# Kernel tuning notes

Measured on AMD Instinct MI355X. Metric: run time of the kernel, lower is better.

## Reference

```python
import jax, jax.numpy as jnp
import numpy as np

DIM = 512
HEADS = 8
DIM_HEAD = 64
INNER = HEADS * DIM_HEAD  # 512
SCALE = DIM_HEAD ** -0.5
NEG = -jnp.finfo(jnp.float32).max


def setup_inputs() -> dict:
    key = jax.random.key(0)
    k1, k2, k3, k4, k5 = jax.random.split(key, 5)
    b, n = 2, 4096
    x = jax.random.normal(k1, (b, n, DIM), dtype=jnp.float32)
    mask = jnp.ones((b, n), dtype=bool)
    gamma = jnp.ones((DIM,), dtype=jnp.float32)
    # nn.Linear default init ~ U(-1/sqrt(fan_in), 1/sqrt(fan_in)); use scaled normal for simplicity
    Wq = jax.random.normal(k2, (DIM, INNER), dtype=jnp.float32) * (DIM ** -0.5)
    Wkv = jax.random.normal(k3, (DIM, 2 * INNER), dtype=jnp.float32) * (DIM ** -0.5)
    Wout = jax.random.normal(k4, (INNER, DIM), dtype=jnp.float32) * (INNER ** -0.5)
    return {"x": x, "mask": mask, "gamma": gamma, "Wq": Wq, "Wkv": Wkv, "Wout": Wout}


def _layer_norm(x, gamma):
    mu = jnp.mean(x, axis=-1, keepdims=True)
    var = jnp.var(x, axis=-1, keepdims=True)
    return (x - mu) * jax.lax.rsqrt(var + 1e-5) * gamma  # beta buffer is zeros


def reference(x, mask, gamma, Wq, Wkv, Wout):
    b, n, _ = x.shape
    xn = _layer_norm(x, gamma)
    q = xn @ Wq                      # [b,n,inner]
    kv = xn @ Wkv                    # [b,n,2*inner]
    k, v = jnp.split(kv, 2, axis=-1)
    # b n (h d) -> b h n d
    def split_heads(t):
        return t.reshape(b, n, HEADS, DIM_HEAD).transpose(0, 2, 1, 3)
    q, k, v = split_heads(q) * SCALE, split_heads(k), split_heads(v)
    sim = jnp.einsum('bhid,bhjd->bhij', q, k)  # [b,h,n,n]
    sim = jnp.where(mask[:, None, None, :], sim, NEG)
    causal = jnp.triu(jnp.ones((n, n), dtype=bool), k=1)
    sim = jnp.where(causal, NEG, sim)
    attn = jax.nn.softmax(sim, axis=-1)
    out = jnp.einsum('bhij,bhjd->bhid', attn, v)       # [b,h,n,d]
    out = out.transpose(0, 2, 1, 3).reshape(b, n, INNER)
    return out @ Wout
```

## Files before the change

kernel.cpp:

```cpp
#include <hip/hip_runtime.h>
#include <hip/hip_bf16.h>
#include <stdint.h>

typedef __attribute__((ext_vector_type(8))) short bf16x8;
typedef __attribute__((ext_vector_type(4))) float f32x4;
typedef __attribute__((ext_vector_type(16))) float f32x16;
typedef __attribute__((ext_vector_type(4))) uint32_t u32x4;

__device__ __forceinline__ short f2bf(float f) {
    union { float f; uint32_t u; } v; v.f = f;
    uint32_t r = v.u + 0x7fffu + ((v.u >> 16) & 1u);
    return (short)(r >> 16);
}

__device__ __forceinline__ float bf2f(uint32_t bits) {
    union { uint32_t u; float f; } v; v.u = bits;
    return v.f;
}

__device__ __forceinline__ uint32_t cvtpk(float a, float b) {
    uint32_t r;
    asm("v_cvt_pk_bf16_f32 %0, %1, %2" : "=v"(r) : "v"(a), "v"(b));
    return r;
}

__device__ __forceinline__ void plswap(uint32_t& x, uint32_t& y) {
    asm volatile("v_permlane32_swap_b32 %0, %1" : "+v"(x), "+v"(y));
}

__device__ __forceinline__ f32x16 mfma32(bf16x8 a, bf16x8 b, f32x16 c) {
    return __builtin_amdgcn_mfma_f32_32x32x16_bf16(a, b, c, 0, 0, 0);
}

__device__ __forceinline__ void gload_lds16(const void* g, void* l) {
    __builtin_amdgcn_global_load_lds(
        (const __attribute__((address_space(1))) void*)g,
        (__attribute__((address_space(3))) void*)l, 16, 0, 0);
}

__global__ __launch_bounds__(256) void prep_weights(
    const float* __restrict__ Wq, const float* __restrict__ Wkv,
    const float* __restrict__ Wout, short* __restrict__ WqkvT,
    short* __restrict__ WoutT) {
    int tid = blockIdx.x * 256 + threadIdx.x;
    if (tid < 1536 * 512) {
        int n = tid >> 9, k = tid & 511;
        float w = (n < 512) ? Wq[k * 512 + n] : Wkv[k * 1024 + (n - 512)];
        WqkvT[tid] = f2bf(w);
    } else {
        int t = tid - 1536 * 512;
        int n = t >> 9, k = t & 511;
        WoutT[t] = f2bf(Wout[k * 512 + n]);
    }
}

__global__ __launch_bounds__(256) void layernorm_k(
    const float* __restrict__ x, const float* __restrict__ gamma,
    short* __restrict__ xn) {
    int row = blockIdx.x;
    const float* xr = x + (size_t)row * 512;
    float2 v = *(const float2*)(xr + threadIdx.x * 2);
    float s = v.x + v.y;
    float ss = v.x * v.x + v.y * v.y;
#pragma unroll
    for (int off = 1; off < 64; off <<= 1) {
        s += __shfl_xor(s, off);
        ss += __shfl_xor(ss, off);
    }
    __shared__ float sbuf[4], ssbuf[4];
    int wid = threadIdx.x >> 6;
    if ((threadIdx.x & 63) == 0) { sbuf[wid] = s; ssbuf[wid] = ss; }
    __syncthreads();
    s = sbuf[0] + sbuf[1] + sbuf[2] + sbuf[3];
    ss = ssbuf[0] + ssbuf[1] + ssbuf[2] + ssbuf[3];
    float mu = s * (1.f / 512.f);
    float var = ss * (1.f / 512.f) - mu * mu;
    float rstd = rsqrtf(var + 1e-5f);
    float2 g = *(const float2*)(gamma + threadIdx.x * 2);
    uint32_t lo = (uint16_t)f2bf((v.x - mu) * rstd * g.x);
    uint32_t hi = (uint16_t)f2bf((v.y - mu) * rstd * g.y);
    *(uint32_t*)(xn + (size_t)row * 512 + threadIdx.x * 2) = lo | (hi << 16);
}

template <int EPI>
__global__ __launch_bounds__(256) void gemm_bt(const short* __restrict__ A,
                                               const short* __restrict__ Bt,
                                               void* __restrict__ C) {
    constexpr int K = 512;
    constexpr int CS = (EPI == 0) ? 1536 : 512;
    __shared__ __align__(16) short As[128 * 64];
    __shared__ __align__(16) short Bs[128 * 64];
    const int tid = threadIdx.x;
    const int lane = tid & 63;
    const int wid = tid >> 6;
    const int m0 = blockIdx.x * 128;
    const int n0 = blockIdx.y * 128;
    const int wr = wid >> 1, wc = wid & 1;
    const int hi = lane >> 4, lo = lane & 15;

    f32x4 acc[4][4] = {};
    for (int kt = 0; kt < K / 64; ++kt) {
        __syncthreads();
#pragma unroll
        for (int r = 0; r < 4; ++r) {
            int c = (r * 4 + wid) * 64 + lane;
            int row = c >> 3, c8 = c & 7;
            int kcol = kt * 64 + ((c8 ^ (row & 7)) << 3);
            gload_lds16(A + (size_t)(m0 + row) * K + kcol,
                        (char*)As + (r * 4 + wid) * 1024);
            gload_lds16(Bt + (size_t)(n0 + row) * K + kcol,
                        (char*)Bs + (r * 4 + wid) * 1024);
        }
        __syncthreads();
#pragma unroll
        for (int kk = 0; kk < 2; ++kk) {
            bf16x8 af[4], bfr[4];
            int cc = hi + kk * 4;
#pragma unroll
            for (int i = 0; i < 4; ++i) {
                int row = wr * 64 + i * 16 + lo;
                af[i] = *(const bf16x8*)((const char*)As + row * 128 +
                                         ((cc ^ (row & 7)) << 4));
                int nrow = wc * 64 + i * 16 + lo;
                bfr[i] = *(const bf16x8*)((const char*)Bs + nrow * 128 +
                                          ((cc ^ (nrow & 7)) << 4));
            }
#pragma unroll
            for (int i = 0; i < 4; ++i)
#pragma unroll
                for (int j = 0; j < 4; ++j)
                    acc[i][j] = __builtin_amdgcn_mfma_f32_16x16x32_bf16(
                        af[i], bfr[j], acc[i][j], 0, 0, 0);
        }
    }
#pragma unroll
    for (int i = 0; i < 4; ++i)
#pragma unroll
        for (int j = 0; j < 4; ++j) {
            int col = n0 + wc * 64 + j * 16 + lo;
#pragma unroll
            for (int r = 0; r < 4; ++r) {
                int row = m0 + wr * 64 + i * 16 + hi * 4 + r;
                float v = acc[i][j][r];
                if (EPI == 0) {
                    if (col < 512) v *= 0.18033688011112042f;
                    ((short*)C)[(size_t)row * CS + col] = f2bf(v);
                } else {
                    ((float*)C)[(size_t)row * CS + col] = v;
                }
            }
        }
}

__global__ __launch_bounds__(256) void transpose_v(const short* __restrict__ qkv,
                                                   short* __restrict__ Vt) {
    __shared__ __align__(16) short T[64 * 72];
    int tid = threadIdx.x;
    int bh = blockIdx.y, b = bh >> 3, h = bh & 7;
    int n0 = blockIdx.x * 64;
    const short* src = qkv + (size_t)(b * 4096 + n0) * 1536 + 1024 + h * 64;
#pragma unroll
    for (int r = 0; r < 2; ++r) {
        int c = r * 256 + tid;
        int t = c >> 3, d0 = (c & 7) * 8;
        *(bf16x8*)(&T[t * 72 + d0]) = *(const bf16x8*)(src + (size_t)t * 1536 + d0);
    }
    __syncthreads();
    short* dst = Vt + (size_t)bh * 64 * 4096 + n0;
#pragma unroll
    for (int r = 0; r < 2; ++r) {
        int c = r * 256 + tid;
        int d = c >> 3, tt0 = (c & 7) * 8;
        short o[8];
#pragma unroll
        for (int j = 0; j < 8; ++j) o[j] = T[(tt0 + j) * 72 + d];
        *(bf16x8*)(dst + (size_t)d * 4096 + tt0) = *(bf16x8*)o;
    }
}

__global__ __launch_bounds__(256, 4) void flash_attn(
    const short* __restrict__ qkv, const short* __restrict__ Vt,
    short* __restrict__ attn_out) {
    __shared__ __align__(16) char smem[32768];
    const int tid = threadIdx.x, lane = tid & 63, w = tid >> 6;
    const int hi32 = lane >> 5, lq = lane & 31;
    const int bid = blockIdx.x;
    const int qt = 127 - (bid >> 4);
    const int bh = bid & 15, b = bh >> 3, h = bh & 7;
    const int q0 = qt * 32;
    const int qg = q0 + lq;
    const int swzK = (lq & 7) ^ ((lq >> 3) & 1);
    const int swzV = (lq >> 1) & 3;

    bf16x8 qb[4];
    {
        const short* qrow = qkv + (size_t)(b * 4096 + qg) * 1536 + h * 64;
#pragma unroll
        for (int ks = 0; ks < 4; ++ks)
            qb[ks] = *(const bf16x8*)(qrow + ks * 16 + hi32 * 8);
    }

    const short* kptr = qkv + (size_t)b * 4096 * 1536 + 512 + h * 64;
    const short* vptr = Vt + (size_t)bh * 64 * 4096;
    char* mybuf = smem + w * 8192;

    auto stage = [&](int t) {
        const short* kp = kptr + (size_t)t * 32 * 1536;
        const short* vp = vptr + t * 32;
#pragma unroll
        for (int r = 0; r < 4; ++r) {
            int idx = r * 64 + lane;
            int krow = idx >> 3, kc = idx & 7;
            int ksw = (krow & 7) ^ ((krow >> 3) & 1);
            gload_lds16(kp + (size_t)krow * 1536 + ((kc ^ ksw) << 3),
                        mybuf + idx * 16);
            int vrow = idx >> 2, vc = idx & 3;
            int vcl = vc ^ ((vrow >> 1) & 3);
            gload_lds16(vp + (size_t)vrow * 4096 + (vcl << 3),
                        mybuf + 4096 + idx * 16);
        }
    };

    f32x16 oA = {}, oB = {};
    float m_r = -3.0e38f, l_r = 0.f;
    const int T = qt + 1;

    if (w < T) {
        stage(w);
        for (int t = w; t < T; t += 4) {
            asm volatile("s_waitcnt vmcnt(0)" ::: "memory");
            f32x16 sA = {};
            __builtin_amdgcn_s_setprio(1);
#pragma unroll
            for (int ks = 0; ks < 4; ++ks) {
                int p = (2 * ks + hi32) ^ swzK;
                bf16x8 kf = *(const bf16x8*)(mybuf + lq * 128 + p * 16);
                sA = mfma32(kf, qb[ks], sA);
            }
            __builtin_amdgcn_s_setprio(0);
            bf16x8 vfA[2], vfB[2];
#pragma unroll
            for (int ks = 0; ks < 2; ++ks) {
                int p = (2 * ks + hi32) ^ swzV;
                vfA[ks] = *(const bf16x8*)(mybuf + 4096 + lq * 64 + p * 16);
                vfB[ks] =
                    *(const bf16x8*)(mybuf + 4096 + (lq + 32) * 64 + p * 16);
            }
            asm volatile("s_waitcnt lgkmcnt(0)" ::: "memory");
            __builtin_amdgcn_sched_barrier(0);
            if (t + 4 < T) stage(t + 4);
            int kv0 = t * 32;
            if (kv0 + 31 > q0) {
                int c4 = 4 * hi32;
#pragma unroll
                for (int r2 = 0; r2 < 16; ++r2) {
                    int kvl = (r2 & 3) + 8 * (r2 >> 2) + c4;
                    sA[r2] = (kv0 + kvl > qg) ? -3.0e38f : sA[r2];
                }
            }
            float m0 = m_r, m1 = m_r, m2 = m_r, m3 = m_r;
#pragma unroll
            for (int r2 = 0; r2 < 16; r2 += 4) {
                m0 = fmaxf(sA[r2], m0);
                m1 = fmaxf(sA[r2 + 1], m1);
                m2 = fmaxf(sA[r2 + 2], m2);
                m3 = fmaxf(sA[r2 + 3], m3);
            }
            float mt = fmaxf(fmaxf(m0, m1), fmaxf(m2, m3));
            mt = fmaxf(mt, __shfl_xor(mt, 32));
            if (!__all(mt <= m_r + 8.0f)) {
                float alpha = exp2f(m_r - mt);
                m_r = mt;
                l_r *= alpha;
#pragma unroll
                for (int r2 = 0; r2 < 16; ++r2) {
                    oA[r2] *= alpha;
                    oB[r2] *= alpha;
                }
            }
            float sum0 = 0.f;
#pragma unroll
            for (int r2 = 0; r2 < 16; ++r2) {
                sA[r2] = exp2f(sA[r2] - m_r);
                sum0 += sA[r2];
            }
            float rs = sum0 + __shfl_xor(sum0, 32);
            l_r += rs;
#pragma unroll
            for (int ks = 0; ks < 2; ++ks) {
                const int base = ks * 8;
                uint32_t x0 = cvtpk(sA[base + 0], sA[base + 1]);
                uint32_t y0 = cvtpk(sA[base + 4], sA[base + 5]);
                plswap(x0, y0);
                uint32_t x1 = cvtpk(sA[base + 2], sA[base + 3]);
                uint32_t y1 = cvtpk(sA[base + 6], sA[base + 7]);
                plswap(x1, y1);
                union { uint32_t wd[4]; bf16x8 v; } u;
                u.wd[0] = x0; u.wd[1] = x1; u.wd[2] = y0; u.wd[3] = y1;
                __builtin_amdgcn_s_setprio(1);
                oA = mfma32(vfA[ks], u.v, oA);
                oB = mfma32(vfB[ks], u.v, oB);
                __builtin_amdgcn_s_setprio(0);
            }
        }
    }
    __syncthreads();
    {
        char* epi = smem + w * 4352;
        float invl = (l_r > 0.f) ? (1.0f / l_r) : 0.f;
#pragma unroll
        for (int r2 = 0; r2 < 16; r2 += 2) {
            int wbase = ((r2 & 3) >> 1) + 4 * (r2 >> 2) + 2 * hi32;
            *(uint32_t*)(epi + lq * 136 + wbase * 4) =
                cvtpk(oA[r2] * invl, oA[r2 + 1] * invl);
            *(uint32_t*)(epi + lq * 136 + 64 + wbase * 4) =
                cvtpk(oB[r2] * invl, oB[r2 + 1] * invl);
        }
        float* mlb = (float*)(smem + 17408);
        if (hi32 == 0) {
            mlb[w * 64 + lq] = m_r;
            mlb[w * 64 + 32 + lq] = l_r;
        }
    }
    __syncthreads();
    {
        const int q = tid >> 3, dg = tid & 7;
        const float* mlb = (const float*)(smem + 17408);
        float M = -3.0e38f;
        float mm[4], ll[4];
#pragma unroll
        for (int s = 0; s < 4; ++s) {
            mm[s] = mlb[s * 64 + q];
            ll[s] = mlb[s * 64 + 32 + q];
            M = fmaxf(M, mm[s]);
        }
        float L = 0.f;
        float acc[8] = {};
#pragma unroll
        for (int s = 0; s < 4; ++s) {
            float a = exp2f(mm[s] - M) * ll[s];
            L += a;
            u32x4 pv = *(const u32x4*)(smem + s * 4352 + q * 136 + dg * 16);
#pragma unroll
            for (int j = 0; j < 4; ++j) {
                acc[2 * j] += a * bf2f(pv[j] << 16);
                acc[2 * j + 1] += a * bf2f(pv[j] & 0xffff0000u);
            }
        }
        float inv = 1.0f / L;
        u32x4 o;
#pragma unroll
        for (int j = 0; j < 4; ++j)
            o[j] = cvtpk(acc[2 * j] * inv, acc[2 * j + 1] * inv);
        uint32_t* attn32 = (uint32_t*)attn_out;
        *(u32x4*)(attn32 + (size_t)(b * 4096 + q0 + q) * 256 + h * 32 + dg * 4) =
            o;
    }
}

extern "C" void kernel_launch(void* const* d_in, const int* in_sizes, int n_in,
                              void* d_out, int out_size, void* d_ws,
                              size_t ws_size, hipStream_t stream) {
    const float* x = (const float*)d_in[0];
    const float* gamma = (const float*)d_in[2];
    const float* Wq = (const float*)d_in[3];
    const float* Wkv = (const float*)d_in[4];
    const float* Wout = (const float*)d_in[5];

    char* ws = (char*)d_ws;
    short* xn = (short*)(ws);
    short* qkv = (short*)(ws + (8ull << 20));
    short* Vt = (short*)(ws + (32ull << 20));
    short* attn = (short*)(ws + (40ull << 20));
    short* WqkvT = (short*)(ws + (48ull << 20));
    short* WoutT = (short*)(ws + (50ull << 20));

    prep_weights<<<4096, 256, 0, stream>>>(Wq, Wkv, Wout, WqkvT, WoutT);
    layernorm_k<<<8192, 256, 0, stream>>>(x, gamma, xn);
    gemm_bt<0><<<dim3(64, 12), 256, 0, stream>>>(xn, WqkvT, qkv);
    transpose_v<<<dim3(64, 16), 256, 0, stream>>>(qkv, Vt);
    flash_attn<<<2048, 256, 0, stream>>>(qkv, Vt, attn);
    gemm_bt<1><<<dim3(64, 4), 256, 0, stream>>>(attn, WoutT, (float*)d_out);
}
```

Measured before the change: 133.7 us.

## Fuse layernorm with weight prep, write V transposed from QKV GEMM, streamline softmax

Merges weight conversion and layernorm into one launch, and has the QKV GEMM epilogue write V directly in transposed layout, which removes the separate transpose kernel and two launches. The attention kernel precomputes its staging offsets and seeds scores with the negated running max so the max subtraction folds into the MFMA accumulator init. It also restructures the online-softmax rescale and sum reductions and shrinks the epilogue LDS stride from 136 to 132 bytes. The transposed V stores are 8-byte scattered writes, which may be less coalesced than the old transpose kernel's output.

```diff
diff --git a/kernel.cpp b/kernel.cpp
--- a/kernel.cpp
+++ b/kernel.cpp
@@ -3,6 +3,7 @@
 #include <stdint.h>
 
 typedef __attribute__((ext_vector_type(8))) short bf16x8;
+typedef __attribute__((ext_vector_type(4))) short s16x4;
 typedef __attribute__((ext_vector_type(4))) float f32x4;
 typedef __attribute__((ext_vector_type(16))) float f32x16;
 typedef __attribute__((ext_vector_type(4))) uint32_t u32x4;
@@ -38,56 +39,55 @@
         (__attribute__((address_space(3))) void*)l, 16, 0, 0);
 }
 
-__global__ __launch_bounds__(256) void prep_weights(
+__global__ __launch_bounds__(256) void prep_ln(
+    const float* __restrict__ x, const float* __restrict__ gamma,
     const float* __restrict__ Wq, const float* __restrict__ Wkv,
-    const float* __restrict__ Wout, short* __restrict__ WqkvT,
-    short* __restrict__ WoutT) {
-    int tid = blockIdx.x * 256 + threadIdx.x;
-    if (tid < 1536 * 512) {
-        int n = tid >> 9, k = tid & 511;
-        float w = (n < 512) ? Wq[k * 512 + n] : Wkv[k * 1024 + (n - 512)];
-        WqkvT[tid] = f2bf(w);
+    const float* __restrict__ Wout, short* __restrict__ xn,
+    short* __restrict__ WqkvT, short* __restrict__ WoutT) {
+    if (blockIdx.x < 8192) {
+        int row = blockIdx.x;
+        const float* xr = x + (size_t)row * 512;
+        float2 v = *(const float2*)(xr + threadIdx.x * 2);
+        float s = v.x + v.y;
+        float ss = v.x * v.x + v.y * v.y;
+#pragma unroll
+        for (int off = 1; off < 64; off <<= 1) {
+            s += __shfl_xor(s, off);
+            ss += __shfl_xor(ss, off);
+        }
+        __shared__ float sbuf[4], ssbuf[4];
+        int wid = threadIdx.x >> 6;
+        if ((threadIdx.x & 63) == 0) { sbuf[wid] = s; ssbuf[wid] = ss; }
+        __syncthreads();
+        s = sbuf[0] + sbuf[1] + sbuf[2] + sbuf[3];
+        ss = ssbuf[0] + ssbuf[1] + ssbuf[2] + ssbuf[3];
+        float mu = s * (1.f / 512.f);
+        float var = ss * (1.f / 512.f) - mu * mu;
+        float rstd = rsqrtf(var + 1e-5f);
+        float2 g = *(const float2*)(gamma + threadIdx.x * 2);
+        uint32_t lo = (uint16_t)f2bf((v.x - mu) * rstd * g.x);
+        uint32_t hi = (uint16_t)f2bf((v.y - mu) * rstd * g.y);
+        *(uint32_t*)(xn + (size_t)row * 512 + threadIdx.x * 2) = lo | (hi << 16);
     } else {
-        int t = tid - 1536 * 512;
-        int n = t >> 9, k = t & 511;
-        WoutT[t] = f2bf(Wout[k * 512 + n]);
-    }
-}
-
-__global__ __launch_bounds__(256) void layernorm_k(
-    const float* __restrict__ x, const float* __restrict__ gamma,
-    short* __restrict__ xn) {
-    int row = blockIdx.x;
-    const float* xr = x + (size_t)row * 512;
-    float2 v = *(const float2*)(xr + threadIdx.x * 2);
-    float s = v.x + v.y;
-    float ss = v.x * v.x + v.y * v.y;
-#pragma unroll
-    for (int off = 1; off < 64; off <<= 1) {
-        s += __shfl_xor(s, off);
-        ss += __shfl_xor(ss, off);
-    }
-    __shared__ float sbuf[4], ssbuf[4];
-    int wid = threadIdx.x >> 6;
-    if ((threadIdx.x & 63) == 0) { sbuf[wid] = s; ssbuf[wid] = ss; }
-    __syncthreads();
-    s = sbuf[0] + sbuf[1] + sbuf[2] + sbuf[3];
-    ss = ssbuf[0] + ssbuf[1] + ssbuf[2] + ssbuf[3];
-    float mu = s * (1.f / 512.f);
-    float var = ss * (1.f / 512.f) - mu * mu;
-    float rstd = rsqrtf(var + 1e-5f);
-    float2 g = *(const float2*)(gamma + threadIdx.x * 2);
-    uint32_t lo = (uint16_t)f2bf((v.x - mu) * rstd * g.x);
-    uint32_t hi = (uint16_t)f2bf((v.y - mu) * rstd * g.y);
-    *(uint32_t*)(xn + (size_t)row * 512 + threadIdx.x * 2) = lo | (hi << 16);
+        int tid = (blockIdx.x - 8192) * 256 + threadIdx.x;
+        if (tid < 1536 * 512) {
+            int n = tid >> 9, k = tid & 511;
+            float w = (n < 512) ? Wq[k * 512 + n] : Wkv[k * 1024 + (n - 512)];
+            WqkvT[tid] = f2bf(w);
+        } else {
+            int t = tid - 1536 * 512;
+            int n = t >> 9, k = t & 511;
+            WoutT[t] = f2bf(Wout[k * 512 + n]);
+        }
+    }
 }
 
 template <int EPI>
 __global__ __launch_bounds__(256) void gemm_bt(const short* __restrict__ A,
                                                const short* __restrict__ Bt,
-                                               void* __restrict__ C) {
+                                               void* __restrict__ C,
+                                               short* __restrict__ Vt) {
     constexpr int K = 512;
-    constexpr int CS = (EPI == 0) ? 1536 : 512;
     __shared__ __align__(16) short As[128 * 64];
     __shared__ __align__(16) short Bs[128 * 64];
     const int tid = threadIdx.x;
@@ -138,44 +138,28 @@
 #pragma unroll
         for (int j = 0; j < 4; ++j) {
             int col = n0 + wc * 64 + j * 16 + lo;
-#pragma unroll
-            for (int r = 0; r < 4; ++r) {
-                int row = m0 + wr * 64 + i * 16 + hi * 4 + r;
-                float v = acc[i][j][r];
-                if (EPI == 0) {
-                    if (col < 512) v *= 0.18033688011112042f;
-                    ((short*)C)[(size_t)row * CS + col] = f2bf(v);
-                } else {
-                    ((float*)C)[(size_t)row * CS + col] = v;
-                }
-            }
-        }
-}
-
-__global__ __launch_bounds__(256) void transpose_v(const short* __restrict__ qkv,
-                                                   short* __restrict__ Vt) {
-    __shared__ __align__(16) short T[64 * 72];
-    int tid = threadIdx.x;
-    int bh = blockIdx.y, b = bh >> 3, h = bh & 7;
-    int n0 = blockIdx.x * 64;
-    const short* src = qkv + (size_t)(b * 4096 + n0) * 1536 + 1024 + h * 64;
-#pragma unroll
-    for (int r = 0; r < 2; ++r) {
-        int c = r * 256 + tid;
-        int t = c >> 3, d0 = (c & 7) * 8;
-        *(bf16x8*)(&T[t * 72 + d0]) = *(const bf16x8*)(src + (size_t)t * 1536 + d0);
-    }
-    __syncthreads();
-    short* dst = Vt + (size_t)bh * 64 * 4096 + n0;
-#pragma unroll
-    for (int r = 0; r < 2; ++r) {
-        int c = r * 256 + tid;
-        int d = c >> 3, tt0 = (c & 7) * 8;
-        short o[8];
-#pragma unroll
-        for (int j = 0; j < 8; ++j) o[j] = T[(tt0 + j) * 72 + d];
-        *(bf16x8*)(dst + (size_t)d * 4096 + tt0) = *(bf16x8*)o;
-    }
+            int row0 = m0 + wr * 64 + i * 16 + hi * 4;
+            if (EPI == 1) {
+#pragma unroll
+                for (int r = 0; r < 4; ++r)
+                    ((float*)C)[(size_t)(row0 + r) * 512 + col] = acc[i][j][r];
+            } else if (col < 1024) {
+                float sc = (col < 512) ? 0.18033688011112042f : 1.0f;
+#pragma unroll
+                for (int r = 0; r < 4; ++r)
+                    ((short*)C)[(size_t)(row0 + r) * 1536 + col] =
+                        f2bf(acc[i][j][r] * sc);
+            } else {
+                s16x4 pk;
+#pragma unroll
+                for (int r = 0; r < 4; ++r) pk[r] = f2bf(acc[i][j][r]);
+                int d = col - 1024;
+                int bb = row0 >> 12, n = row0 & 4095;
+                *(s16x4*)(Vt + ((size_t)(bb * 8 + (d >> 6)) * 64 + (d & 63)) *
+                                   4096 +
+                          n) = pk;
+            }
+        }
 }
 
 __global__ __launch_bounds__(256, 4) void flash_attn(
@@ -200,36 +184,39 @@
             qb[ks] = *(const bf16x8*)(qrow + ks * 16 + hi32 * 8);
     }
 
-    const short* kptr = qkv + (size_t)b * 4096 * 1536 + 512 + h * 64;
-    const short* vptr = Vt + (size_t)bh * 64 * 4096;
+    int offK[4], offV[4], ldsO[4];
+#pragma unroll
+    for (int r = 0; r < 4; ++r) {
+        int idx = r * 64 + lane;
+        int krow = idx >> 3, kc = idx & 7;
+        int ksw = (krow & 7) ^ ((krow >> 3) & 1);
+        offK[r] = krow * 1536 + ((kc ^ ksw) << 3);
+        int vrow = idx >> 2, vc = idx & 3;
+        offV[r] = vrow * 4096 + ((vc ^ ((vrow >> 1) & 3)) << 3);
+        ldsO[r] = idx * 16;
+    }
     char* mybuf = smem + w * 8192;
-
-    auto stage = [&](int t) {
-        const short* kp = kptr + (size_t)t * 32 * 1536;
-        const short* vp = vptr + t * 32;
+    const short* kps =
+        qkv + (size_t)b * 4096 * 1536 + 512 + h * 64 + (size_t)w * 32 * 1536;
+    const short* vps = Vt + (size_t)bh * 64 * 4096 + w * 32;
+
+    f32x16 oA = {}, oB = {};
+    float m_r = 0.f, l_r = 0.f;
+    const int T = qt + 1;
+
+    if (w < T) {
 #pragma unroll
         for (int r = 0; r < 4; ++r) {
-            int idx = r * 64 + lane;
-            int krow = idx >> 3, kc = idx & 7;
-            int ksw = (krow & 7) ^ ((krow >> 3) & 1);
-            gload_lds16(kp + (size_t)krow * 1536 + ((kc ^ ksw) << 3),
-                        mybuf + idx * 16);
-            int vrow = idx >> 2, vc = idx & 3;
-            int vcl = vc ^ ((vrow >> 1) & 3);
-            gload_lds16(vp + (size_t)vrow * 4096 + (vcl << 3),
-                        mybuf + 4096 + idx * 16);
-        }
-    };
-
-    f32x16 oA = {}, oB = {};
-    float m_r = -3.0e38f, l_r = 0.f;
-    const int T = qt + 1;
-
-    if (w < T) {
-        stage(w);
+            gload_lds16(kps + offK[r], mybuf + ldsO[r]);
+            gload_lds16(vps + offV[r], mybuf + 4096 + ldsO[r]);
+        }
+        kps += (size_t)4 * 32 * 1536;
+        vps += 4 * 32;
         for (int t = w; t < T; t += 4) {
             asm volatile("s_waitcnt vmcnt(0)" ::: "memory");
-            f32x16 sA = {};
+            f32x16 sA;
+#pragma unroll
+            for (int r2 = 0; r2 < 16; ++r2) sA[r2] = -m_r;
             __builtin_amdgcn_s_setprio(1);
 #pragma unroll
             for (int ks = 0; ks < 4; ++ks) {
@@ -248,7 +235,15 @@
             }
             asm volatile("s_waitcnt lgkmcnt(0)" ::: "memory");
             __builtin_amdgcn_sched_barrier(0);
-            if (t + 4 < T) stage(t + 4);
+            if (t + 4 < T) {
+#pragma unroll
+                for (int r = 0; r < 4; ++r) {
+                    gload_lds16(kps + offK[r], mybuf + ldsO[r]);
+                    gload_lds16(vps + offV[r], mybuf + 4096 + ldsO[r]);
+                }
+                kps += (size_t)4 * 32 * 1536;
+                vps += 4 * 32;
+            }
             int kv0 = t * 32;
             if (kv0 + 31 > q0) {
                 int c4 = 4 * hi32;
@@ -258,34 +253,39 @@
                     sA[r2] = (kv0 + kvl > qg) ? -3.0e38f : sA[r2];
                 }
             }
-            float m0 = m_r, m1 = m_r, m2 = m_r, m3 = m_r;
-#pragma unroll
-            for (int r2 = 0; r2 < 16; r2 += 4) {
-                m0 = fmaxf(sA[r2], m0);
-                m1 = fmaxf(sA[r2 + 1], m1);
-                m2 = fmaxf(sA[r2 + 2], m2);
-                m3 = fmaxf(sA[r2 + 3], m3);
-            }
-            float mt = fmaxf(fmaxf(m0, m1), fmaxf(m2, m3));
+            float a0 = fmaxf(fmaxf(sA[0], sA[1]), sA[2]);
+            float a1 = fmaxf(fmaxf(sA[3], sA[4]), sA[5]);
+            float a2 = fmaxf(fmaxf(sA[6], sA[7]), sA[8]);
+            float a3 = fmaxf(fmaxf(sA[9], sA[10]), sA[11]);
+            float a4 = fmaxf(fmaxf(sA[12], sA[13]), sA[14]);
+            float mt = fmaxf(fmaxf(fmaxf(a0, a1), a2),
+                             fmaxf(fmaxf(a3, a4), sA[15]));
             mt = fmaxf(mt, __shfl_xor(mt, 32));
-            if (!__all(mt <= m_r + 8.0f)) {
-                float alpha = exp2f(m_r - mt);
-                m_r = mt;
+            float sum0;
+            if (!__all(mt <= 8.0f)) {
+                float dm = fmaxf(mt, 0.f);
+                float alpha = exp2f(-dm);
+                m_r += dm;
                 l_r *= alpha;
 #pragma unroll
                 for (int r2 = 0; r2 < 16; ++r2) {
                     oA[r2] *= alpha;
                     oB[r2] *= alpha;
                 }
-            }
-            float sum0 = 0.f;
-#pragma unroll
-            for (int r2 = 0; r2 < 16; ++r2) {
-                sA[r2] = exp2f(sA[r2] - m_r);
-                sum0 += sA[r2];
-            }
-            float rs = sum0 + __shfl_xor(sum0, 32);
-            l_r += rs;
+#pragma unroll
+                for (int r2 = 0; r2 < 16; ++r2) sA[r2] = exp2f(sA[r2] - dm);
+            } else {
+#pragma unroll
+                for (int r2 = 0; r2 < 16; ++r2) sA[r2] = exp2f(sA[r2]);
+            }
+            {
+                float s0 = (sA[0] + sA[1]) + (sA[2] + sA[3]);
+                float s1 = (sA[4] + sA[5]) + (sA[6] + sA[7]);
+                float s2 = (sA[8] + sA[9]) + (sA[10] + sA[11]);
+                float s3 = (sA[12] + sA[13]) + (sA[14] + sA[15]);
+                sum0 = (s0 + s1) + (s2 + s3);
+            }
+            l_r += sum0 + __shfl_xor(sum0, 32);
 #pragma unroll
             for (int ks = 0; ks < 2; ++ks) {
                 const int base = ks * 8;
@@ -306,17 +306,17 @@
     }
     __syncthreads();
     {
-        char* epi = smem + w * 4352;
+        char* epi = smem + w * 4224;
         float invl = (l_r > 0.f) ? (1.0f / l_r) : 0.f;
 #pragma unroll
         for (int r2 = 0; r2 < 16; r2 += 2) {
             int wbase = ((r2 & 3) >> 1) + 4 * (r2 >> 2) + 2 * hi32;
-            *(uint32_t*)(epi + lq * 136 + wbase * 4) =
+            *(uint32_t*)(epi + lq * 132 + wbase * 4) =
                 cvtpk(oA[r2] * invl, oA[r2 + 1] * invl);
-            *(uint32_t*)(epi + lq * 136 + 64 + wbase * 4) =
+            *(uint32_t*)(epi + lq * 132 + 64 + wbase * 4) =
                 cvtpk(oB[r2] * invl, oB[r2 + 1] * invl);
         }
-        float* mlb = (float*)(smem + 17408);
+        float* mlb = (float*)(smem + 16896);
         if (hi32 == 0) {
             mlb[w * 64 + lq] = m_r;
             mlb[w * 64 + 32 + lq] = l_r;
@@ -325,7 +325,7 @@
     __syncthreads();
     {
         const int q = tid >> 3, dg = tid & 7;
-        const float* mlb = (const float*)(smem + 17408);
+        const float* mlb = (const float*)(smem + 16896);
         float M = -3.0e38f;
         float mm[4], ll[4];
 #pragma unroll
@@ -340,11 +340,13 @@
         for (int s = 0; s < 4; ++s) {
             float a = exp2f(mm[s] - M) * ll[s];
             L += a;
-            u32x4 pv = *(const u32x4*)(smem + s * 4352 + q * 136 + dg * 16);
+            const uint32_t* p32 =
+                (const uint32_t*)(smem + s * 4224 + q * 132 + dg * 16);
 #pragma unroll
             for (int j = 0; j < 4; ++j) {
-                acc[2 * j] += a * bf2f(pv[j] << 16);
-                acc[2 * j + 1] += a * bf2f(pv[j] & 0xffff0000u);
+                uint32_t pv = p32[j];
+                acc[2 * j] += a * bf2f(pv << 16);
+                acc[2 * j + 1] += a * bf2f(pv & 0xffff0000u);
             }
         }
         float inv = 1.0f / L;
@@ -375,10 +377,10 @@
     short* WqkvT = (short*)(ws + (48ull << 20));
     short* WoutT = (short*)(ws + (50ull << 20));
 
-    prep_weights<<<4096, 256, 0, stream>>>(Wq, Wkv, Wout, WqkvT, WoutT);
-    layernorm_k<<<8192, 256, 0, stream>>>(x, gamma, xn);
-    gemm_bt<0><<<dim3(64, 12), 256, 0, stream>>>(xn, WqkvT, qkv);
-    transpose_v<<<dim3(64, 16), 256, 0, stream>>>(qkv, Vt);
+    prep_ln<<<12288, 256, 0, stream>>>(x, gamma, Wq, Wkv, Wout, xn, WqkvT,
+                                       WoutT);
+    gemm_bt<0><<<dim3(64, 12), 256, 0, stream>>>(xn, WqkvT, qkv, Vt);
     flash_attn<<<2048, 256, 0, stream>>>(qkv, Vt, attn);
-    gemm_bt<1><<<dim3(64, 4), 256, 0, stream>>>(attn, WoutT, (float*)d_out);
-}
+    gemm_bt<1><<<dim3(64, 4), 256, 0, stream>>>(attn, WoutT, (float*)d_out,
+                                                nullptr);
+}
```

After: 359.5 us. 2.69x slower.
